# Kernel optimization log

Hardware: AMD Instinct MI355X
Metric: run time of the kernel (lower is better)

## Reference

```python
import jax, jax.numpy as jnp
import numpy as np

N_NODES = 50000
N_EDGES = 800000
NFEAT, NHID, NCLASS = 512, 128, 40


def _glorot(key, fan_in, fan_out):
    # mimics the usual GCN uniform init: U(-1/sqrt(fan_out), 1/sqrt(fan_out))
    stdv = 1.0 / np.sqrt(fan_out)
    return jax.random.uniform(key, (fan_in, fan_out), jnp.float32, -stdv, stdv)


def setup_inputs() -> dict:
    key = jax.random.key(0)
    ks = jax.random.split(key, 8)
    x = jax.random.normal(ks[0], (N_NODES, NFEAT), jnp.float32)
    edge_src = jax.random.randint(ks[1], (N_EDGES,), 0, N_NODES)
    edge_dst = jax.random.randint(ks[2], (N_EDGES,), 0, N_NODES)
    edge_weight = jax.random.uniform(ks[3], (N_EDGES,), jnp.float32)
    W1 = _glorot(ks[4], NFEAT, NHID)
    b1 = jnp.zeros((NHID,), jnp.float32)
    W2 = _glorot(ks[5], NHID, NCLASS)
    b2 = jnp.zeros((NCLASS,), jnp.float32)
    return {"x": x, "edge_src": edge_src, "edge_dst": edge_dst,
            "edge_weight": edge_weight, "W1": W1, "b1": b1, "W2": W2, "b2": b2}


def _gcn_layer(x, W, b, edge_src, edge_dst, edge_weight):
    # support = x @ W ; out = spmm(adj, support) + b
    support = x @ W                                   # [N, F_out]
    msgs = support[edge_src] * edge_weight[:, None]   # [E, F_out]
    agg = jax.ops.segment_sum(msgs, edge_dst, num_segments=N_NODES)
    return agg + b


def reference(x, edge_src, edge_dst, edge_weight, W1, b1, W2, b2):
    h = _gcn_layer(x, W1, b1, edge_src, edge_dst, edge_weight)
    h = jax.nn.relu(h)
    # F.dropout(training=False) -> identity in eval mode
    out = _gcn_layer(h, W2, b2, edge_src, edge_dst, edge_weight)
    return out
```

## Files before the change

### kernel.cpp

```cpp
#include <hip/hip_runtime.h>


#define F0 512
#define F1 128
#define F2 40
#define F2P 48

typedef short bf16x8 __attribute__((ext_vector_type(8)));
typedef float f32x4 __attribute__((ext_vector_type(4)));

static __device__ __forceinline__ unsigned short f2b(float f){
    union { float f; unsigned int u; } x; x.f = f;
    unsigned int u = x.u;
    unsigned int r = (u + 0x7fffu + ((u >> 16) & 1u)) >> 16;
    return (unsigned short)r;
}
static __device__ __forceinline__ unsigned short f2b_fast(float f){
    return (unsigned short)((__float_as_uint(f) + 0x8000u) >> 16);
}
static __device__ __forceinline__ unsigned int pack2(float a, float b){
    unsigned int ua = __float_as_uint(a) + 0x8000u;
    unsigned int ub = __float_as_uint(b) + 0x8000u;
    return __builtin_amdgcn_perm(ub, ua, 0x07060302u);
}
static __device__ __forceinline__ bf16x8 pack8(float4 v0, float4 v1){
    union { bf16x8 v; unsigned int d[4]; } r;
    r.d[0] = pack2(v0.x, v0.y);
    r.d[1] = pack2(v0.z, v0.w);
    r.d[2] = pack2(v1.x, v1.y);
    r.d[3] = pack2(v1.z, v1.w);
    return r.v;
}
static __device__ __forceinline__ float b2f(unsigned short h){
    union { unsigned int u; float f; } x; x.u = ((unsigned int)h) << 16; return x.f;
}
static __device__ __forceinline__ unsigned short f2h(float f){
    union { _Float16 h; unsigned short u; } x; x.h = (_Float16)f; return x.u;
}
static __device__ __forceinline__ float h2f(unsigned short u){
    union { unsigned short u; _Float16 h; } x; x.u = u; return (float)x.h;
}

__global__ void hist_kernel(const int* __restrict__ dst, int* __restrict__ cnt, int E){
    int e = blockIdx.x*256 + threadIdx.x;
    if (e < E) atomicAdd(&cnt[dst[e]], 1);
}

__global__ void scan1_kernel(const int* __restrict__ cnt, int* __restrict__ offs,
                             int* __restrict__ bsum, int n){
    __shared__ int sd[256];
    int tid = threadIdx.x;
    int base = blockIdx.x*1024 + tid*4;
    int c0 = (base+0<n)?cnt[base+0]:0;
    int c1 = (base+1<n)?cnt[base+1]:0;
    int c2 = (base+2<n)?cnt[base+2]:0;
    int c3 = (base+3<n)?cnt[base+3]:0;
    int v1=c0, v2=c0+c1, v3=c0+c1+c2;
    int s = c0+c1+c2+c3;
    sd[tid]=s; __syncthreads();
    for (int off=1; off<256; off<<=1){
        int t = (tid>=off)? sd[tid-off] : 0;
        __syncthreads();
        sd[tid] += t;
        __syncthreads();
    }
    int excl = sd[tid] - s;
    if (base+0<n) offs[base+0]=excl;
    if (base+1<n) offs[base+1]=excl+v1;
    if (base+2<n) offs[base+2]=excl+v2;
    if (base+3<n) offs[base+3]=excl+v3;
    if (tid==255) bsum[blockIdx.x]=sd[255];
}

__global__ void scan3_kernel(int* __restrict__ offs, int* __restrict__ cur,
                             const int* __restrict__ bsum, int n, int E, int nb){
    __shared__ int sexcl;
    int tid = threadIdx.x;
    if (tid < 64){
        int v = (tid < nb) ? bsum[tid] : 0;
        int orig = v;
        #pragma unroll
        for (int off=1; off<64; off<<=1){
            int t = __shfl_up(v, off);
            if (tid >= off) v += t;
        }
        int g = blockIdx.x >> 2;
        if (tid == g) sexcl = v - orig;
    }
    __syncthreads();
    int i = blockIdx.x*256 + tid;
    if (i<n){ int o = offs[i] + sexcl; offs[i]=o; cur[i]=o; }
    if (i==0) offs[n]=E;
}

__global__ void scatter_kernel(const int* __restrict__ src, const int* __restrict__ dst,
                               const float* __restrict__ w, int* __restrict__ cur,
                               unsigned int* __restrict__ edges, int E){
    int e = blockIdx.x*256+threadIdx.x;
    if (e<E){
        int d = dst[e];
        int pos = atomicAdd(&cur[d],1);
        edges[pos] = ((unsigned int)src[e] << 16) | (unsigned int)f2h(w[e]);
    }
}

__global__ void prep_w(const float* __restrict__ W1, const float* __restrict__ W2,
                       unsigned short* __restrict__ W1t, unsigned short* __restrict__ W2t){
    int idx = blockIdx.x*256 + threadIdx.x;
    if (idx < F0*F1){
        int k = idx >> 7, n = idx & 127;
        W1t[(size_t)n*F0 + k] = f2b(W1[idx]);
    } else {
        int j = idx - F0*F1;
        if (j < F2P*F1){
            int n = j >> 7, k = j & 127;
            float v = (n < F2) ? W2[(size_t)k*F2 + n] : 0.f;
            W2t[j] = f2b(v);
        }
    }
}

__global__ __launch_bounds__(256) void gemm1_mfma(const float* __restrict__ X,
                                                  const unsigned short* __restrict__ W1t,
                                                  unsigned short* __restrict__ S1, int M){
    __shared__ unsigned short sB[128][72];
    int tid = threadIdx.x;
    int wave = tid >> 6, lane = tid & 63;
    int quad = lane >> 4, l16 = lane & 15;
    int row0 = blockIdx.x * 64;
    int myrow = row0 + wave*16 + l16;
    int arow = min(myrow, M-1);
    const float* xrow = X + (size_t)arow * F0;

    int sn = tid >> 1, shalf = tid & 1;
    const unsigned short* bsrc = W1t + (size_t)sn*F0 + shalf*32;
    unsigned short* bdst = &sB[sn][shalf*32];

    f32x4 acc[8];
    #pragma unroll
    for (int c=0;c<8;c++) acc[c] = (f32x4){0.f,0.f,0.f,0.f};

    float4 a0 = *(const float4*)(xrow + quad*8);
    float4 a1 = *(const float4*)(xrow + quad*8 + 4);
    float4 a2 = *(const float4*)(xrow + 32 + quad*8);
    float4 a3 = *(const float4*)(xrow + 32 + quad*8 + 4);
    {
        float4 b0 = *(const float4*)(bsrc+ 0), b1 = *(const float4*)(bsrc+ 8);
        float4 b2 = *(const float4*)(bsrc+16), b3 = *(const float4*)(bsrc+24);
        *(float4*)(bdst+ 0)=b0; *(float4*)(bdst+ 8)=b1;
        *(float4*)(bdst+16)=b2; *(float4*)(bdst+24)=b3;
    }
    __syncthreads();

    for (int k0 = 0; k0 < F0; k0 += 64){
        bool more = (k0 + 64) < F0;
        float4 na0, na1, na2, na3, nb0, nb1, nb2, nb3;
        if (more){
            const float* nx = xrow + k0 + 64;
            na0 = *(const float4*)(nx + quad*8);
            na1 = *(const float4*)(nx + quad*8 + 4);
            na2 = *(const float4*)(nx + 32 + quad*8);
            na3 = *(const float4*)(nx + 32 + quad*8 + 4);
            const unsigned short* p = bsrc + k0 + 64;
            nb0 = *(const float4*)(p+ 0); nb1 = *(const float4*)(p+ 8);
            nb2 = *(const float4*)(p+16); nb3 = *(const float4*)(p+24);
        }
        bf16x8 af0 = pack8(a0, a1);
        bf16x8 af1 = pack8(a2, a3);
        #pragma unroll
        for (int c=0;c<8;c++){
            bf16x8 b0 = *(bf16x8*)&sB[c*16 + l16][quad*8];
            bf16x8 b1 = *(bf16x8*)&sB[c*16 + l16][32 + quad*8];
            acc[c] = __builtin_amdgcn_mfma_f32_16x16x32_bf16(af0, b0, acc[c], 0, 0, 0);
            acc[c] = __builtin_amdgcn_mfma_f32_16x16x32_bf16(af1, b1, acc[c], 0, 0, 0);
        }
        if (more){
            __syncthreads();
            *(float4*)(bdst+ 0)=nb0; *(float4*)(bdst+ 8)=nb1;
            *(float4*)(bdst+16)=nb2; *(float4*)(bdst+24)=nb3;
            __syncthreads();
            a0 = na0; a1 = na1; a2 = na2; a3 = na3;
        }
    }
    #pragma unroll
    for (int c=0;c<8;c++){
        #pragma unroll
        for (int r=0;r<4;r++){
            int grow = row0 + wave*16 + quad*4 + r;
            if (grow < M) S1[(size_t)grow*F1 + c*16 + l16] = f2b_fast(acc[c][r]);
        }
    }
}

__global__ void agg1_kernel(const unsigned short* __restrict__ S1, const int* __restrict__ offs,
                            const unsigned int* __restrict__ edges,
                            const float* __restrict__ b1, unsigned short* __restrict__ H, int n){
    int node = blockIdx.x*4 + (threadIdx.x >> 6);
    int lane = threadIdx.x & 63;
    if (node >= n) return;
    int half = lane >> 5, fl = lane & 31;
    int e0 = offs[node], e1 = offs[node+1];
    double a0=0.0, a1=0.0, a2=0.0, a3=0.0;
    int e = e0;
    for (; e+8 <= e1; e += 8){
        unsigned int rA = edges[e   + half];
        unsigned int rB = edges[e+2 + half];
        unsigned int rC = edges[e+4 + half];
        unsigned int rD = edges[e+6 + half];
        ushort4 vA = *(const ushort4*)&S1[((size_t)(rA>>16))*F1 + fl*4];
        ushort4 vB = *(const ushort4*)&S1[((size_t)(rB>>16))*F1 + fl*4];
        ushort4 vC = *(const ushort4*)&S1[((size_t)(rC>>16))*F1 + fl*4];
        ushort4 vD = *(const ushort4*)&S1[((size_t)(rD>>16))*F1 + fl*4];
        double wA = h2f((unsigned short)rA), wB = h2f((unsigned short)rB);
        double wC = h2f((unsigned short)rC), wD = h2f((unsigned short)rD);
        a0 += wA*b2f(vA.x) + wB*b2f(vB.x) + wC*b2f(vC.x) + wD*b2f(vD.x);
        a1 += wA*b2f(vA.y) + wB*b2f(vB.y) + wC*b2f(vC.y) + wD*b2f(vD.y);
        a2 += wA*b2f(vA.z) + wB*b2f(vB.z) + wC*b2f(vC.z) + wD*b2f(vD.z);
        a3 += wA*b2f(vA.w) + wB*b2f(vB.w) + wC*b2f(vC.w) + wD*b2f(vD.w);
    }
    for (; e < e1; e += 2){
        int ee = e + half;
        if (ee < e1){
            unsigned int r = edges[ee];
            ushort4 v = *(const ushort4*)&S1[((size_t)(r>>16))*F1 + fl*4];
            double w = h2f((unsigned short)r);
            a0 += w*b2f(v.x); a1 += w*b2f(v.y); a2 += w*b2f(v.z); a3 += w*b2f(v.w);
        }
    }
    a0 += __shfl_down(a0, 32);
    a1 += __shfl_down(a1, 32);
    a2 += __shfl_down(a2, 32);
    a3 += __shfl_down(a3, 32);
    if (lane < 32){
        float4 bb = *(const float4*)&b1[fl*4];
        float o0 = (float)(a0 + (double)bb.x);
        float o1 = (float)(a1 + (double)bb.y);
        float o2 = (float)(a2 + (double)bb.z);
        float o3 = (float)(a3 + (double)bb.w);
        o0 = o0>0.f?o0:0.f; o1 = o1>0.f?o1:0.f;
        o2 = o2>0.f?o2:0.f; o3 = o3>0.f?o3:0.f;
        union { ushort4 v; unsigned int d[2]; } o;
        o.d[0] = pack2(o0, o1);
        o.d[1] = pack2(o2, o3);
        *(ushort4*)&H[(size_t)node*F1 + fl*4] = o.v;
    }
}

__global__ __launch_bounds__(256) void gemm2_mfma(const unsigned short* __restrict__ H,
                                                  const unsigned short* __restrict__ W2t,
                                                  unsigned short* __restrict__ S2, int M){
    __shared__ unsigned short sB[48][136];
    int tid = threadIdx.x;
    int wave = tid >> 6, lane = tid & 63;
    int quad = lane >> 4, l16 = lane & 15;
    for (int i = tid; i < 48*16; i += 256){
        int nn = i >> 4, p = i & 15;
        *(float4*)&sB[nn][p*8] = *(const float4*)&W2t[(size_t)nn*F1 + p*8];
    }
    int row0 = blockIdx.x * 64;
    int myrow = row0 + wave*16 + l16;
    int arow = min(myrow, M-1);
    const unsigned short* hrow = H + (size_t)arow * F1;
    bf16x8 a[4];
    #pragma unroll
    for (int ks=0; ks<4; ks++) a[ks] = *(const bf16x8*)(hrow + ks*32 + quad*8);
    __syncthreads();
    f32x4 acc[3];
    #pragma unroll
    for (int c=0;c<3;c++) acc[c] = (f32x4){0.f,0.f,0.f,0.f};
    #pragma unroll
    for (int ks=0; ks<4; ks++){
        #pragma unroll
        for (int c=0;c<3;c++){
            bf16x8 b = *(bf16x8*)&sB[c*16 + l16][ks*32 + quad*8];
            acc[c] = __builtin_amdgcn_mfma_f32_16x16x32_bf16(a[ks], b, acc[c], 0, 0, 0);
        }
    }
    #pragma unroll
    for (int c=0;c<3;c++){
        #pragma unroll
        for (int r=0;r<4;r++){
            int grow = row0 + wave*16 + quad*4 + r;
            if (grow < M) S2[(size_t)grow*F2P + c*16 + l16] = f2b_fast(acc[c][r]);
        }
    }
}

__global__ void agg2_kernel(const unsigned short* __restrict__ S2, const int* __restrict__ offs,
                            const unsigned int* __restrict__ edges,
                            const float* __restrict__ b2, float* __restrict__ out, int n){
    int node = blockIdx.x*4 + (threadIdx.x >> 6);
    int lane = threadIdx.x & 63;
    if (node >= n) return;
    int grp = lane >> 4, gl = lane & 15;
    bool act = gl < 10;
    int e0 = offs[node], e1 = offs[node+1];
    double a0=0.0, a1=0.0, a2=0.0, a3=0.0;
    for (int e = e0; e < e1; e += 4){
        int ee = e + grp;
        if (ee < e1 && act){
            unsigned int r = edges[ee];
            ushort4 v = *(const ushort4*)&S2[((size_t)(r>>16))*F2P + gl*4];
            double w = h2f((unsigned short)r);
            a0 += w*b2f(v.x); a1 += w*b2f(v.y); a2 += w*b2f(v.z); a3 += w*b2f(v.w);
        }
    }
    a0 += __shfl_down(a0, 32); a0 += __shfl_down(a0, 16);
    a1 += __shfl_down(a1, 32); a1 += __shfl_down(a1, 16);
    a2 += __shfl_down(a2, 32); a2 += __shfl_down(a2, 16);
    a3 += __shfl_down(a3, 32); a3 += __shfl_down(a3, 16);
    if (lane < 10){
        float4 bb = *(const float4*)&b2[lane*4];
        float4 o;
        o.x = (float)(a0 + (double)bb.x);
        o.y = (float)(a1 + (double)bb.y);
        o.z = (float)(a2 + (double)bb.z);
        o.w = (float)(a3 + (double)bb.w);
        *(float4*)&out[(size_t)node*F2 + lane*4] = o;
    }
}

extern "C" void kernel_launch(void* const* d_in, const int* in_sizes, int n_in,
                              void* d_out, int out_size, void* d_ws, size_t ws_size,
                              hipStream_t stream){
    const float* x    = (const float*)d_in[0];
    const int*   esrc = (const int*)d_in[1];
    const int*   edst = (const int*)d_in[2];
    const float* ew   = (const float*)d_in[3];
    const float* W1   = (const float*)d_in[4];
    const float* b1   = (const float*)d_in[5];
    const float* W2   = (const float*)d_in[6];
    const float* b2   = (const float*)d_in[7];
    float* out = (float*)d_out;
    int N = in_sizes[0] / F0;
    int E = in_sizes[1];

    char* ws = (char*)d_ws;
    size_t off = 0;
    auto alloc = [&](size_t bytes)->void*{
        void* p = ws + off; off += (bytes + 255) & ~(size_t)255; return p;
    };
    unsigned short* S1 = (unsigned short*)alloc(sizeof(unsigned short)*(size_t)N*F1);
    unsigned short* H  = (unsigned short*)alloc(sizeof(unsigned short)*(size_t)N*F1);
    unsigned short* S2 = (unsigned short*)alloc(sizeof(unsigned short)*(size_t)N*F2P);
    unsigned short* W1t = (unsigned short*)alloc(sizeof(unsigned short)*F1*F0);
    unsigned short* W2t = (unsigned short*)alloc(sizeof(unsigned short)*F2P*F1);
    int*   offs  = (int*)alloc(sizeof(int)*(size_t)(N+1));
    int*   cur   = (int*)alloc(sizeof(int)*(size_t)N);
    unsigned int* edges = (unsigned int*)alloc(sizeof(unsigned int)*(size_t)E);
    int*   bsum  = (int*)alloc(sizeof(int)*64);

    hipMemsetAsync(cur, 0, sizeof(int)*(size_t)N, stream);
    hist_kernel<<<(E+255)/256,256,0,stream>>>(edst, cur, E);
    int nb = (N+1023)/1024;
    scan1_kernel<<<nb,256,0,stream>>>(cur, offs, bsum, N);
    scan3_kernel<<<(N+255)/256,256,0,stream>>>(offs, cur, bsum, N, E, nb);
    scatter_kernel<<<(E+255)/256,256,0,stream>>>(esrc, edst, ew, cur, edges, E);

    prep_w<<<(F0*F1 + F2P*F1 + 255)/256,256,0,stream>>>(W1, W2, W1t, W2t);

    gemm1_mfma<<<(N+63)/64,256,0,stream>>>(x, W1t, S1, N);
    agg1_kernel<<<(N+3)/4,256,0,stream>>>(S1, offs, edges, b1, H, N);
    gemm2_mfma<<<(N+63)/64,256,0,stream>>>(H, W2t, S2, N);
    agg2_kernel<<<(N+3)/4,256,0,stream>>>(S2, offs, edges, b2, out, N);
}
```

Measured before the change: 344.6 us.

## Split CSR counters into 8 sub-slots, drop scatter atomics, retile gemm1 over K=128

The CSR build now keeps 8 counters per destination node, chosen by edge index, which spreads atomic contention. Each edge records its slot during the histogram, so the scatter step computes positions directly instead of doing a second atomic pass. Counter zeroing is folded into the weight-prep kernel, which removes the memset. gemm1 now stages 128-wide K chunks of W1 in shared memory with padding, cutting barrier count, at the cost of more LDS use and extra count/slot buffers.

```diff
diff --git a/kernel.cpp b/kernel.cpp
--- a/kernel.cpp
+++ b/kernel.cpp
@@ -41,27 +41,69 @@
     union { unsigned short u; _Float16 h; } x; x.u = u; return (float)x.h;
 }
 
-__global__ void hist_kernel(const int* __restrict__ dst, int* __restrict__ cnt, int E){
+__global__ void prep_w(const float* __restrict__ W1, const float* __restrict__ W2,
+                       unsigned short* __restrict__ W1t, unsigned short* __restrict__ W2t,
+                       int* __restrict__ cnt8, int n8){
+    int idx = blockIdx.x*256 + threadIdx.x;
+    if (idx < n8) cnt8[idx] = 0;
+    if (idx < F0*F1){
+        int k = idx >> 7, n = idx & 127;
+        W1t[(size_t)n*F0 + k] = f2b(W1[idx]);
+    } else if (idx < F0*F1 + F2P*F1){
+        int j = idx - F0*F1;
+        int n = j >> 7, k = j & 127;
+        float v = (n < F2) ? W2[(size_t)k*F2 + n] : 0.f;
+        W2t[j] = f2b(v);
+    }
+}
+
+__global__ void hist_kernel(const int* __restrict__ dst, int* __restrict__ cnt8,
+                            unsigned short* __restrict__ slot, int E){
     int e = blockIdx.x*256 + threadIdx.x;
-    if (e < E) atomicAdd(&cnt[dst[e]], 1);
-}
-
-__global__ void scan1_kernel(const int* __restrict__ cnt, int* __restrict__ offs,
-                             int* __restrict__ bsum, int n){
+    if (e < E){
+        int d = dst[e];
+        int s = e & 7;
+        slot[e] = (unsigned short)atomicAdd(&cnt8[d*8 + s], 1);
+    }
+}
+
+__global__ void scan1_kernel(const int* __restrict__ cnt8, int* __restrict__ offs,
+                             unsigned short* __restrict__ lsp, int* __restrict__ bsum, int n){
     __shared__ int sd[256];
     int tid = threadIdx.x;
     int base = blockIdx.x*1024 + tid*4;
-    int c0 = (base+0<n)?cnt[base+0]:0;
-    int c1 = (base+1<n)?cnt[base+1]:0;
-    int c2 = (base+2<n)?cnt[base+2]:0;
-    int c3 = (base+3<n)?cnt[base+3]:0;
-    int v1=c0, v2=c0+c1, v3=c0+c1+c2;
-    int s = c0+c1+c2+c3;
+    int t[4];
+    #pragma unroll
+    for (int j=0;j<4;j++){
+        int node = base+j;
+        int tot = 0;
+        if (node < n){
+            int4 c0 = *(const int4*)&cnt8[(size_t)node*8];
+            int4 c1 = *(const int4*)&cnt8[(size_t)node*8+4];
+            unsigned short lp0=0, lp1, lp2, lp3, lp4, lp5, lp6, lp7;
+            int run = c0.x; lp1=(unsigned short)run;
+            run += c0.y; lp2=(unsigned short)run;
+            run += c0.z; lp3=(unsigned short)run;
+            run += c0.w; lp4=(unsigned short)run;
+            run += c1.x; lp5=(unsigned short)run;
+            run += c1.y; lp6=(unsigned short)run;
+            run += c1.z; lp7=(unsigned short)run;
+            run += c1.w; tot = run;
+            ushort4 a, b;
+            a.x=lp0; a.y=lp1; a.z=lp2; a.w=lp3;
+            b.x=lp4; b.y=lp5; b.z=lp6; b.w=lp7;
+            *(ushort4*)&lsp[(size_t)node*8]   = a;
+            *(ushort4*)&lsp[(size_t)node*8+4] = b;
+        }
+        t[j] = tot;
+    }
+    int v1=t[0], v2=t[0]+t[1], v3=v2+t[2];
+    int s = v3+t[3];
     sd[tid]=s; __syncthreads();
     for (int off=1; off<256; off<<=1){
-        int t = (tid>=off)? sd[tid-off] : 0;
+        int tt = (tid>=off)? sd[tid-off] : 0;
         __syncthreads();
-        sd[tid] += t;
+        sd[tid] += tt;
         __syncthreads();
     }
     int excl = sd[tid] - s;
@@ -72,7 +114,8 @@
     if (tid==255) bsum[blockIdx.x]=sd[255];
 }
 
-__global__ void scan3_kernel(int* __restrict__ offs, int* __restrict__ cur,
+__global__ void scan3_kernel(int* __restrict__ offs, int* __restrict__ sbase,
+                             const unsigned short* __restrict__ lsp,
                              const int* __restrict__ bsum, int n, int E, int nb){
     __shared__ int sexcl;
     int tid = threadIdx.x;
@@ -89,41 +132,37 @@
     }
     __syncthreads();
     int i = blockIdx.x*256 + tid;
-    if (i<n){ int o = offs[i] + sexcl; offs[i]=o; cur[i]=o; }
+    if (i<n){
+        int o = offs[i] + sexcl;
+        offs[i] = o;
+        ushort4 a = *(const ushort4*)&lsp[(size_t)i*8];
+        ushort4 b = *(const ushort4*)&lsp[(size_t)i*8+4];
+        int4 s0, s1;
+        s0.x=o+a.x; s0.y=o+a.y; s0.z=o+a.z; s0.w=o+a.w;
+        s1.x=o+b.x; s1.y=o+b.y; s1.z=o+b.z; s1.w=o+b.w;
+        *(int4*)&sbase[(size_t)i*8]   = s0;
+        *(int4*)&sbase[(size_t)i*8+4] = s1;
+    }
     if (i==0) offs[n]=E;
 }
 
 __global__ void scatter_kernel(const int* __restrict__ src, const int* __restrict__ dst,
-                               const float* __restrict__ w, int* __restrict__ cur,
+                               const float* __restrict__ w,
+                               const int* __restrict__ sbase,
+                               const unsigned short* __restrict__ slot,
                                unsigned int* __restrict__ edges, int E){
     int e = blockIdx.x*256+threadIdx.x;
     if (e<E){
         int d = dst[e];
-        int pos = atomicAdd(&cur[d],1);
+        int pos = sbase[d*8 + (e & 7)] + (int)slot[e];
         edges[pos] = ((unsigned int)src[e] << 16) | (unsigned int)f2h(w[e]);
-    }
-}
-
-__global__ void prep_w(const float* __restrict__ W1, const float* __restrict__ W2,
-                       unsigned short* __restrict__ W1t, unsigned short* __restrict__ W2t){
-    int idx = blockIdx.x*256 + threadIdx.x;
-    if (idx < F0*F1){
-        int k = idx >> 7, n = idx & 127;
-        W1t[(size_t)n*F0 + k] = f2b(W1[idx]);
-    } else {
-        int j = idx - F0*F1;
-        if (j < F2P*F1){
-            int n = j >> 7, k = j & 127;
-            float v = (n < F2) ? W2[(size_t)k*F2 + n] : 0.f;
-            W2t[j] = f2b(v);
-        }
     }
 }
 
 __global__ __launch_bounds__(256) void gemm1_mfma(const float* __restrict__ X,
                                                   const unsigned short* __restrict__ W1t,
                                                   unsigned short* __restrict__ S1, int M){
-    __shared__ unsigned short sB[128][72];
+    __shared__ unsigned short sB[128*136];
     int tid = threadIdx.x;
     int wave = tid >> 6, lane = tid & 63;
     int quad = lane >> 4, l16 = lane & 15;
@@ -132,54 +171,48 @@
     int arow = min(myrow, M-1);
     const float* xrow = X + (size_t)arow * F0;
 
-    int sn = tid >> 1, shalf = tid & 1;
-    const unsigned short* bsrc = W1t + (size_t)sn*F0 + shalf*32;
-    unsigned short* bdst = &sB[sn][shalf*32];
-
     f32x4 acc[8];
     #pragma unroll
     for (int c=0;c<8;c++) acc[c] = (f32x4){0.f,0.f,0.f,0.f};
 
-    float4 a0 = *(const float4*)(xrow + quad*8);
-    float4 a1 = *(const float4*)(xrow + quad*8 + 4);
-    float4 a2 = *(const float4*)(xrow + 32 + quad*8);
-    float4 a3 = *(const float4*)(xrow + 32 + quad*8 + 4);
-    {
-        float4 b0 = *(const float4*)(bsrc+ 0), b1 = *(const float4*)(bsrc+ 8);
-        float4 b2 = *(const float4*)(bsrc+16), b3 = *(const float4*)(bsrc+24);
-        *(float4*)(bdst+ 0)=b0; *(float4*)(bdst+ 8)=b1;
-        *(float4*)(bdst+16)=b2; *(float4*)(bdst+24)=b3;
-    }
-    __syncthreads();
-
-    for (int k0 = 0; k0 < F0; k0 += 64){
-        bool more = (k0 + 64) < F0;
-        float4 na0, na1, na2, na3, nb0, nb1, nb2, nb3;
-        if (more){
-            const float* nx = xrow + k0 + 64;
-            na0 = *(const float4*)(nx + quad*8);
-            na1 = *(const float4*)(nx + quad*8 + 4);
-            na2 = *(const float4*)(nx + 32 + quad*8);
-            na3 = *(const float4*)(nx + 32 + quad*8 + 4);
-            const unsigned short* p = bsrc + k0 + 64;
-            nb0 = *(const float4*)(p+ 0); nb1 = *(const float4*)(p+ 8);
-            nb2 = *(const float4*)(p+16); nb3 = *(const float4*)(p+24);
-        }
-        bf16x8 af0 = pack8(a0, a1);
-        bf16x8 af1 = pack8(a2, a3);
-        #pragma unroll
-        for (int c=0;c<8;c++){
-            bf16x8 b0 = *(bf16x8*)&sB[c*16 + l16][quad*8];
-            bf16x8 b1 = *(bf16x8*)&sB[c*16 + l16][32 + quad*8];
-            acc[c] = __builtin_amdgcn_mfma_f32_16x16x32_bf16(af0, b0, acc[c], 0, 0, 0);
-            acc[c] = __builtin_amdgcn_mfma_f32_16x16x32_bf16(af1, b1, acc[c], 0, 0, 0);
-        }
-        if (more){
-            __syncthreads();
-            *(float4*)(bdst+ 0)=nb0; *(float4*)(bdst+ 8)=nb1;
-            *(float4*)(bdst+16)=nb2; *(float4*)(bdst+24)=nb3;
-            __syncthreads();
-            a0 = na0; a1 = na1; a2 = na2; a3 = na3;
+    float4 aq[4][2];
+    #pragma unroll
+    for (int s=0;s<4;s++){
+        aq[s][0] = *(const float4*)(xrow + s*32 + quad*8);
+        aq[s][1] = *(const float4*)(xrow + s*32 + quad*8 + 4);
+    }
+
+    for (int p = 0; p < 4; p++){
+        __syncthreads();
+        #pragma unroll
+        for (int i=0;i<8;i++){
+            int idx = tid + i*256;
+            int nn = idx >> 4, c8 = idx & 15;
+            *(float4*)&sB[nn*136 + c8*8] =
+                *(const float4*)&W1t[(size_t)nn*F0 + p*128 + c8*8];
+        }
+        __syncthreads();
+        float4 nq[4][2];
+        if (p < 3){
+            const float* nx = xrow + (p+1)*128;
+            #pragma unroll
+            for (int s=0;s<4;s++){
+                nq[s][0] = *(const float4*)(nx + s*32 + quad*8);
+                nq[s][1] = *(const float4*)(nx + s*32 + quad*8 + 4);
+            }
+        }
+        #pragma unroll
+        for (int s=0;s<4;s++){
+            bf16x8 af = pack8(aq[s][0], aq[s][1]);
+            #pragma unroll
+            for (int c=0;c<8;c++){
+                bf16x8 b = *(bf16x8*)&sB[(c*16 + l16)*136 + s*32 + quad*8];
+                acc[c] = __builtin_amdgcn_mfma_f32_16x16x32_bf16(af, b, acc[c], 0, 0, 0);
+            }
+        }
+        if (p < 3){
+            #pragma unroll
+            for (int s=0;s<4;s++){ aq[s][0]=nq[s][0]; aq[s][1]=nq[s][1]; }
         }
     }
     #pragma unroll
@@ -346,18 +379,22 @@
     unsigned short* W1t = (unsigned short*)alloc(sizeof(unsigned short)*F1*F0);
     unsigned short* W2t = (unsigned short*)alloc(sizeof(unsigned short)*F2P*F1);
     int*   offs  = (int*)alloc(sizeof(int)*(size_t)(N+1));
-    int*   cur   = (int*)alloc(sizeof(int)*(size_t)N);
+    int*   cnt8  = (int*)alloc(sizeof(int)*(size_t)N*8);
+    int*   sbase = (int*)alloc(sizeof(int)*(size_t)N*8);
+    unsigned short* lsp  = (unsigned short*)alloc(sizeof(unsigned short)*(size_t)N*8);
+    unsigned short* slot = (unsigned short*)alloc(sizeof(unsigned short)*(size_t)E);
     unsigned int* edges = (unsigned int*)alloc(sizeof(unsigned int)*(size_t)E);
     int*   bsum  = (int*)alloc(sizeof(int)*64);
 
-    hipMemsetAsync(cur, 0, sizeof(int)*(size_t)N, stream);
-    hist_kernel<<<(E+255)/256,256,0,stream>>>(edst, cur, E);
+    int n8 = N*8;
+    int prep_items = n8 > (F0*F1 + F2P*F1) ? n8 : (F0*F1 + F2P*F1);
+    prep_w<<<(prep_items+255)/256,256,0,stream>>>(W1, W2, W1t, W2t, cnt8, n8);
+
+    hist_kernel<<<(E+255)/256,256,0,stream>>>(edst, cnt8, slot, E);
     int nb = (N+1023)/1024;
-    scan1_kernel<<<nb,256,0,stream>>>(cur, offs, bsum, N);
-    scan3_kernel<<<(N+255)/256,256,0,stream>>>(offs, cur, bsum, N, E, nb);
-    scatter_kernel<<<(E+255)/256,256,0,stream>>>(esrc, edst, ew, cur, edges, E);
-
-    prep_w<<<(F0*F1 + F2P*F1 + 255)/256,256,0,stream>>>(W1, W2, W1t, W2t);
+    scan1_kernel<<<nb,256,0,stream>>>(cnt8, offs, lsp, bsum, N);
+    scan3_kernel<<<(N+255)/256,256,0,stream>>>(offs, sbase, lsp, bsum, N, E, nb);
+    scatter_kernel<<<(E+255)/256,256,0,stream>>>(esrc, edst, ew, sbase, slot, edges, E);
 
     gemm1_mfma<<<(N+63)/64,256,0,stream>>>(x, W1t, S1, N);
     agg1_kernel<<<(N+3)/4,256,0,stream>>>(S1, offs, edges, b1, H, N);
```

After: 322.6 us. 1.07x faster.
